# Performance work log

Measured on AMD Instinct MI355X. Metric: run time of the kernel, lower is better.

The kernel has to match this reference:

```python
import jax, jax.numpy as jnp
import numpy as np

B, N, E = 4, 4096, 16384
D, A_DIM = 256, 64
T, HALF, STEPS, NTYPES = 16, 8, 3, 50


def setup_inputs() -> dict:
    key = jax.random.key(0)
    ks = jax.random.split(key, 16)
    s = 0.02  # small init so repeated DxD matmuls stay stable over 3 steps
    return {
        "annotation_id": jax.random.randint(ks[0], (B, N), 0, NTYPES),
        "src": jax.random.randint(ks[1], (B, E), 0, N),
        "dst": jax.random.randint(ks[2], (B, E), 0, N),
        "etype": jax.random.randint(ks[3], (B, E), 0, HALF),
        "edge_embed": jax.random.normal(ks[4], (T, D * D), jnp.float32) * s,
        "edge_bias": jax.random.normal(ks[5], (T, D), jnp.float32) * s,
        "type_embed": jax.random.normal(ks[6], (NTYPES, A_DIM), jnp.float32) * s,
        "Wr": jax.random.normal(ks[7], (D, 3 * D), jnp.float32) * s,
        "br": jnp.zeros((D,), jnp.float32),
        "Wz": jax.random.normal(ks[8], (D, 3 * D), jnp.float32) * s,
        "bz": jnp.zeros((D,), jnp.float32),
        "Wh": jax.random.normal(ks[9], (D, 3 * D), jnp.float32) * s,
        "bh": jnp.zeros((D,), jnp.float32),
        "Wa": jax.random.normal(ks[10], (1, D + A_DIM), jnp.float32) * s,
        "ba": jnp.zeros((1,), jnp.float32),
        "Wo": jax.random.normal(ks[11], (1, D + A_DIM), jnp.float32) * s,
        "bo": jnp.zeros((1,), jnp.float32),
    }


def reference(annotation_id, src, dst, etype, edge_embed, edge_bias, type_embed,
              Wr, br, Wz, bz, Wh, bh, Wa, ba, Wo, bo):
    # annotation: typeEmbed[id-1] if id>0 else zeros  -> [B, N, A_DIM]
    ann = jnp.where((annotation_id > 0)[..., None],
                    type_embed[jnp.clip(annotation_id - 1, 0, NTYPES - 1)],
                    jnp.zeros((), type_embed.dtype))
    # prop_state: annotation zero-padded to state_dim  -> [B, N, D]
    h = jnp.concatenate([ann, jnp.zeros((B, N, D - A_DIM), ann.dtype)], axis=-1)
    W = edge_embed.reshape(T, D, D)  # per-edge-type DxD matrices

    def step(h):
        # type-major projection: apply every edge-type matrix to every node state
        # P[b, t, n, :] = W[t] @ h[b, n]   -> [B, T, N, D]
        P = jnp.einsum('tij,bnj->btni', W, h)

        def per_graph(Pg, s_, d_, e_):
            # a_out[j]        += W[e] @ h[neighbour] + b[e]
            # a_in[neighbour] += W[e+HALF] @ h[j]   + b[e+HALF]
            m_out = Pg[e_, d_] + edge_bias[e_]            # [E, D]
            m_in = Pg[e_ + HALF, s_] + edge_bias[e_ + HALF]
            a_out = jnp.zeros((N, D), h.dtype).at[s_].add(m_out)
            a_in = jnp.zeros((N, D), h.dtype).at[d_].add(m_in)
            return a_in, a_out

        a_in, a_out = jax.vmap(per_graph)(P, src, dst, etype)
        # GRU-style propagator (dropout_rate = 0 -> identity)
        a = jnp.concatenate([a_in, a_out, h], axis=-1)    # [B, N, 3D]
        r = jax.nn.sigmoid(a @ Wr.T + br)
        z = jax.nn.sigmoid(a @ Wz.T + bz)
        h_hat = jnp.tanh(jnp.concatenate([a_in, a_out, r * h], axis=-1) @ Wh.T + bh)
        return (1.0 - z) * h + z * h_hat

    for _ in range(STEPS):
        h = step(h)

    join = jnp.concatenate([h, ann], axis=-1)             # [B, N, D+A]
    atten = jax.nn.sigmoid(join @ Wa.T + ba)              # [B, N, 1]
    ou = jnp.tanh(join @ Wo.T + bo)                       # [B, N, 1]
    w_sum = jnp.sum((atten * ou).reshape(-1, N), axis=1)  # [B]
    return jax.nn.sigmoid(w_sum)
```

## Files before the change

kernel.cpp:

```cpp
#include <hip/hip_runtime.h>
#include <cstdint>

#define BB 4
#define NN 4096
#define EE 16384
#define DD 256
#define ADIM 64
#define TT 16
#define HALFE 8
#define STEPS 3
#define OSTRIDE 4160
#define MAXTILES 1088
#define MAXM (MAXTILES * 128)

typedef __attribute__((ext_vector_type(8))) short short8;
typedef __attribute__((ext_vector_type(4))) float f32x4;

__device__ __forceinline__ float sigmoidf_(float x) { return 1.0f / (1.0f + __expf(-x)); }

__device__ __forceinline__ unsigned short f2bf(float x) {
    unsigned u = __float_as_uint(x);
    u += 0x7fffu + ((u >> 16) & 1u);
    return (unsigned short)(u >> 16);
}
__device__ __forceinline__ float bf2f(unsigned short b) {
    return __uint_as_float(((unsigned)b) << 16);
}

__global__ void init_kernel(const int* __restrict__ ann_id,
                            const float* __restrict__ type_embed,
                            float* __restrict__ ann, float* __restrict__ h,
                            unsigned short* __restrict__ hbf,
                            unsigned short* __restrict__ Xbf) {
    int idx = blockIdx.x * 256 + threadIdx.x;
    int bn = idx >> 6, q = idx & 63;
    int id = ann_id[bn];
    float4 v = {0.f, 0.f, 0.f, 0.f};
    if (q < 16) {
        if (id > 0) v = ((const float4*)(type_embed + (size_t)(id - 1) * ADIM))[q];
        ((float4*)(ann + (size_t)bn * ADIM))[q] = v;
    }
    ((float4*)(h + (size_t)bn * DD))[q] = v;
    ushort4 o;
    o.x = f2bf(v.x); o.y = f2bf(v.y); o.z = f2bf(v.z); o.w = f2bf(v.w);
    ((ushort4*)(hbf + (size_t)bn * DD))[q] = o;
    ((ushort4*)(Xbf + (size_t)bn * 768 + 512))[q] = o;
}

__global__ void conv_f2b4(const float* __restrict__ in, unsigned short* __restrict__ out) {
    int idx = blockIdx.x * 256 + threadIdx.x;
    float4 v = ((const float4*)in)[idx];
    ushort4 o;
    o.x = f2bf(v.x); o.y = f2bf(v.y); o.z = f2bf(v.z); o.w = f2bf(v.w);
    ((ushort4*)out)[idx] = o;
}

__global__ void build_wcat(const float* __restrict__ Wr, const float* __restrict__ Wz,
                           const float* __restrict__ Wh, unsigned short* __restrict__ W) {
    int idx = blockIdx.x * 256 + threadIdx.x;
    int c = idx / 768, k = idx % 768;
    float v;
    if (c < 256)       v = Wr[c * 768 + k];
    else if (c < 512)  v = Wz[(c - 256) * 768 + k];
    else               v = (k < 512) ? Wh[(c - 512) * 768 + k] : 0.f;
    W[idx] = f2bf(v);
}

__global__ void build_whh(const float* __restrict__ Wh, unsigned short* __restrict__ W) {
    int idx = blockIdx.x * 256 + threadIdx.x;
    int i = idx / 256, k = idx % 256;
    W[idx] = f2bf(Wh[i * 768 + 512 + k]);
}

__global__ void count_kernel(const int* __restrict__ src, const int* __restrict__ dst,
                             int* __restrict__ counts) {
    int idx = blockIdx.x * 256 + threadIdx.x;
    int b = idx >> 14;
    atomicAdd(&counts[(b * 2 + 0) * NN + src[idx]], 1);
    atomicAdd(&counts[(b * 2 + 1) * NN + dst[idx]], 1);
}

__global__ __launch_bounds__(1024) void scan_kernel(const int* __restrict__ counts,
                                                    int* __restrict__ offs,
                                                    int* __restrict__ cursor) {
    __shared__ int lsum[1024];
    int t = threadIdx.x, seg = blockIdx.x;
    int4 v = ((const int4*)(counts + (size_t)seg * NN))[t];
    int s1 = v.x + v.y, s2 = s1 + v.z, s3 = s2 + v.w;
    lsum[t] = s3;
    __syncthreads();
    for (int off = 1; off < 1024; off <<= 1) {
        int tmp = (t >= off) ? lsum[t - off] : 0;
        __syncthreads();
        lsum[t] += tmp;
        __syncthreads();
    }
    int base = lsum[t] - s3;
    int* o = offs + (size_t)seg * OSTRIDE;
    o[4 * t] = base; o[4 * t + 1] = base + v.x; o[4 * t + 2] = base + s1; o[4 * t + 3] = base + s2;
    if (t == 1023) o[4096] = lsum[1023];
    int* c = cursor + (size_t)seg * NN;
    c[4 * t] = base; c[4 * t + 1] = base + v.x; c[4 * t + 2] = base + s1; c[4 * t + 3] = base + s2;
}

__global__ void count2_kernel(const int* __restrict__ et, int* __restrict__ c32) {
    __shared__ int cnt[32];
    int tid = threadIdx.x;
    if (tid < 32) cnt[tid] = 0;
    __syncthreads();
    int idx = blockIdx.x * 256 + tid;
    int b = idx >> 14;
    atomicAdd(&cnt[b * 8 + et[idx]], 1);
    __syncthreads();
    if (tid < 32) atomicAdd(&c32[tid], cnt[tid]);
}

__global__ void scan2_kernel(const int* __restrict__ c32, int* __restrict__ type_cursor,
                             int* __restrict__ tile_type) {
    __shared__ int pad[64];
    int t = threadIdx.x;
    int b = t >> 4, dir = (t >> 3) & 1, tt = t & 7;
    int cnt = c32[b * 8 + tt];
    int padded = ((cnt + 127) >> 7) << 7;
    pad[t] = padded;
    __syncthreads();
    int off = 0;
    for (int k = 0; k < t; ++k) off += pad[k];
    type_cursor[t] = off;
    int t16 = dir * 8 + tt;
    int tile0 = off >> 7;
    for (int k = 0; k < (padded >> 7); ++k) tile_type[tile0 + k] = t16;
}

__global__ void fill2_kernel(const int* __restrict__ src, const int* __restrict__ dst,
                             const int* __restrict__ et, int* __restrict__ type_cursor,
                             int* __restrict__ node_cursor, int* __restrict__ entries,
                             int* __restrict__ idx2) {
    __shared__ int cnt[64];
    __shared__ int bse[64];
    int tid = threadIdx.x;
    if (tid < 64) cnt[tid] = 0;
    __syncthreads();
    int idx = blockIdx.x * 256 + tid;
    int b = idx >> 14;
    int s = src[idx], d = dst[idx], t = et[idx];
    int bin0 = b * 16 + t;
    int bin1 = b * 16 + 8 + t;
    int r0 = atomicAdd(&cnt[bin0], 1);
    int r1 = atomicAdd(&cnt[bin1], 1);
    __syncthreads();
    if (tid < 64) bse[tid] = atomicAdd(&type_cursor[tid], cnt[tid]);
    __syncthreads();
    int p0 = bse[bin0] + r0;
    int p1 = bse[bin1] + r1;
    idx2[p0] = b * NN + d;
    idx2[p1] = b * NN + s;
    int q0 = atomicAdd(&node_cursor[(b * 2 + 0) * NN + s], 1);
    entries[(size_t)(b * 2 + 0) * EE + q0] = (p0 << 4) | t;
    int q1 = atomicAdd(&node_cursor[(b * 2 + 1) * NN + d], 1);
    entries[(size_t)(b * 2 + 1) * EE + q1] = (p1 << 4) | (t + 8);
}

#define GEMM_CORE64(A_, Bt_, K_)                                                        \
    const int tid = threadIdx.x;                                                        \
    const int wv = tid >> 6, lane = tid & 63;                                           \
    const int wr = wv >> 1, wc = wv & 1;                                                \
    const int lr = lane & 15, hi = lane >> 4, rx = lane & 7;                            \
    const int srow = wv * 8 + (lane >> 3);                                              \
    const int scol = ((lane & 7) ^ (lane >> 3)) << 3;                                   \
    const unsigned short* Ag = A_ + (size_t)(r0 + srow) * K_ + scol;                    \
    const unsigned short* Bg = Bt_ + (size_t)(c0 + srow) * K_ + scol;                   \
    char* AsW = (char*)As + wv * 1024;                                                  \
    char* BsW = (char*)Bs + wv * 1024;                                                  \
    f32x4 acc[4][4] = {};                                                               \
    for (int k0 = 0; k0 < K_; k0 += 64) {                                               \
        _Pragma("unroll")                                                               \
        for (int i = 0; i < 4; ++i) {                                                   \
            __builtin_amdgcn_global_load_lds(                                           \
                (const __attribute__((address_space(1))) void*)(Ag + (size_t)(i * 32) * K_ + k0), \
                (__attribute__((address_space(3))) void*)(AsW + i * 4096), 16, 0, 0);   \
            __builtin_amdgcn_global_load_lds(                                           \
                (const __attribute__((address_space(1))) void*)(Bg + (size_t)(i * 32) * K_ + k0), \
                (__attribute__((address_space(3))) void*)(BsW + i * 4096), 16, 0, 0);   \
        }                                                                               \
        __syncthreads();                                                                \
        _Pragma("unroll")                                                               \
        for (int kk = 0; kk < 2; ++kk) {                                                \
            short8 af[4], bfv[4];                                                       \
            _Pragma("unroll")                                                           \
            for (int m = 0; m < 4; ++m) {                                               \
                int R = wr * 64 + m * 16 + lr;                                          \
                af[m] = *(const short8*)((const char*)As + R * 128 + (((kk * 4 + hi) ^ rx) << 4)); \
            }                                                                           \
            _Pragma("unroll")                                                           \
            for (int n = 0; n < 4; ++n) {                                               \
                int R = wc * 64 + n * 16 + lr;                                          \
                bfv[n] = *(const short8*)((const char*)Bs + R * 128 + (((kk * 4 + hi) ^ rx) << 4)); \
            }                                                                           \
            _Pragma("unroll")                                                           \
            for (int m = 0; m < 4; ++m)                                                 \
                _Pragma("unroll")                                                       \
                for (int n = 0; n < 4; ++n)                                             \
                    acc[m][n] = __builtin_amdgcn_mfma_f32_16x16x32_bf16(bfv[n], af[m], acc[m][n], 0, 0, 0); \
        }                                                                               \
        __syncthreads();                                                                \
    }                                                                                   \
    const int erow = r0 + wr * 64 + lr;                                                 \
    const int ecol = c0 + wc * 64 + (hi << 2);

__global__ __launch_bounds__(256) void gemm_msgs(const unsigned short* __restrict__ A,
                                                 const unsigned short* __restrict__ W2,
                                                 const int* __restrict__ idx2,
                                                 const int* __restrict__ tile_type,
                                                 unsigned short* __restrict__ C) {
    __shared__ __align__(16) unsigned short As[128 * 64];
    __shared__ __align__(16) unsigned short Bs[128 * 64];
    const int bid = blockIdx.x;
    const int wg = (bid & 7) * (MAXTILES * 2 / 8) + (bid >> 3);
    const int by = wg >> 1, bx = wg & 1;
    const int t16 = tile_type[by];
    if (t16 < 0) return;
    const int r0 = by << 7, c0 = bx << 7;
    const int tid = threadIdx.x;
    const int wv = tid >> 6, lane = tid & 63;
    const int wr = wv >> 1, wc = wv & 1;
    const int lr = lane & 15, hi = lane >> 4, rx = lane & 7;
    const int srow = wv * 8 + (lane >> 3);
    const int scol = ((lane & 7) ^ (lane >> 3)) << 3;
    int ar[4];
#pragma unroll
    for (int i = 0; i < 4; ++i) ar[i] = idx2[r0 + srow + i * 32];
    const unsigned short* Bt = W2 + (size_t)t16 * (DD * DD);
    const unsigned short* Bg = Bt + (size_t)(c0 + srow) * DD + scol;
    char* AsW = (char*)As + wv * 1024;
    char* BsW = (char*)Bs + wv * 1024;
    f32x4 acc[4][4] = {};
    for (int k0 = 0; k0 < DD; k0 += 64) {
#pragma unroll
        for (int i = 0; i < 4; ++i) {
            __builtin_amdgcn_global_load_lds(
                (const __attribute__((address_space(1))) void*)(A + (size_t)ar[i] * DD + scol + k0),
                (__attribute__((address_space(3))) void*)(AsW + i * 4096), 16, 0, 0);
            __builtin_amdgcn_global_load_lds(
                (const __attribute__((address_space(1))) void*)(Bg + (size_t)(i * 32) * DD + k0),
                (__attribute__((address_space(3))) void*)(BsW + i * 4096), 16, 0, 0);
        }
        __syncthreads();
#pragma unroll
        for (int kk = 0; kk < 2; ++kk) {
            short8 af[4], bfv[4];
#pragma unroll
            for (int m = 0; m < 4; ++m) {
                int R = wr * 64 + m * 16 + lr;
                af[m] = *(const short8*)((const char*)As + R * 128 + (((kk * 4 + hi) ^ rx) << 4));
            }
#pragma unroll
            for (int n = 0; n < 4; ++n) {
                int R = wc * 64 + n * 16 + lr;
                bfv[n] = *(const short8*)((const char*)Bs + R * 128 + (((kk * 4 + hi) ^ rx) << 4));
            }
#pragma unroll
            for (int m = 0; m < 4; ++m)
#pragma unroll
                for (int n = 0; n < 4; ++n)
                    acc[m][n] = __builtin_amdgcn_mfma_f32_16x16x32_bf16(bfv[n], af[m], acc[m][n], 0, 0, 0);
        }
        __syncthreads();
    }
    const int erow = r0 + wr * 64 + lr;
    const int ecol = c0 + wc * 64 + (hi << 2);
#pragma unroll
    for (int m = 0; m < 4; ++m)
#pragma unroll
        for (int n = 0; n < 4; ++n) {
            ushort4 o;
            o.x = f2bf(acc[m][n][0]); o.y = f2bf(acc[m][n][1]);
            o.z = f2bf(acc[m][n][2]); o.w = f2bf(acc[m][n][3]);
            *(ushort4*)&C[(size_t)(erow + m * 16) * DD + ecol + n * 16] = o;
        }
}

__global__ __launch_bounds__(256) void gemm_rzu(const unsigned short* __restrict__ A,
                                                const unsigned short* __restrict__ Bt,
                                                const float* __restrict__ br,
                                                const float* __restrict__ bz,
                                                const float* __restrict__ h,
                                                unsigned short* __restrict__ RH,
                                                unsigned short* __restrict__ Zb,
                                                unsigned short* __restrict__ Ub) {
    __shared__ __align__(16) unsigned short As[128 * 64];
    __shared__ __align__(16) unsigned short Bs[128 * 64];
    const int bid = blockIdx.x;
    const int wg = (bid & 7) * 96 + (bid >> 3);
    const int bx = wg % 6, by = wg / 6;
    const int r0 = by << 7, c0 = bx << 7;
    GEMM_CORE64(A, Bt, 768)
    const int region = c0 >> 8;
#pragma unroll
    for (int m = 0; m < 4; ++m)
#pragma unroll
        for (int n = 0; n < 4; ++n) {
            int gr = erow + m * 16;
            int gc = ecol + n * 16;
            f32x4 v = acc[m][n];
            if (region == 0) {
                float4 bb = *(const float4*)&br[gc];
                float4 hv = *(const float4*)&h[(size_t)gr * 256 + gc];
                ushort4 o;
                o.x = f2bf(sigmoidf_(v[0] + bb.x) * hv.x);
                o.y = f2bf(sigmoidf_(v[1] + bb.y) * hv.y);
                o.z = f2bf(sigmoidf_(v[2] + bb.z) * hv.z);
                o.w = f2bf(sigmoidf_(v[3] + bb.w) * hv.w);
                *(ushort4*)&RH[(size_t)gr * 256 + gc] = o;
            } else if (region == 1) {
                int c = gc - 256;
                float4 bb = *(const float4*)&bz[c];
                ushort4 o;
                o.x = f2bf(sigmoidf_(v[0] + bb.x));
                o.y = f2bf(sigmoidf_(v[1] + bb.y));
                o.z = f2bf(sigmoidf_(v[2] + bb.z));
                o.w = f2bf(sigmoidf_(v[3] + bb.w));
                *(ushort4*)&Zb[(size_t)gr * 256 + c] = o;
            } else {
                int c = gc - 512;
                ushort4 o;
                o.x = f2bf(v[0]); o.y = f2bf(v[1]); o.z = f2bf(v[2]); o.w = f2bf(v[3]);
                *(ushort4*)&Ub[(size_t)gr * 256 + c] = o;
            }
        }
}

__global__ __launch_bounds__(256) void gemm_hh(const unsigned short* __restrict__ A,
                                               const unsigned short* __restrict__ Bt,
                                               const unsigned short* __restrict__ Zb,
                                               const unsigned short* __restrict__ Ub,
                                               const float* __restrict__ bh,
                                               float* __restrict__ h,
                                               unsigned short* __restrict__ hbf,
                                               unsigned short* __restrict__ Xbf) {
    __shared__ __align__(16) unsigned short As[128 * 64];
    __shared__ __align__(16) unsigned short Bs[128 * 64];
    const int bid = blockIdx.x;
    const int wg = (bid & 7) * 32 + (bid >> 3);
    const int bx = wg & 1, by = wg >> 1;
    const int r0 = by << 7, c0 = bx << 7;
    GEMM_CORE64(A, Bt, 256)
#pragma unroll
    for (int m = 0; m < 4; ++m)
#pragma unroll
        for (int n = 0; n < 4; ++n) {
            int gr = erow + m * 16;
            int gc = ecol + n * 16;
            size_t base = (size_t)gr * 256 + gc;
            f32x4 v = acc[m][n];
            float4 bb = *(const float4*)&bh[gc];
            float4 hv = *(const float4*)&h[base];
            ushort4 zp = *(const ushort4*)&Zb[base];
            ushort4 up = *(const ushort4*)&Ub[base];
            float4 hn;
            {
                float z = bf2f(zp.x); hn.x = (1.f - z) * hv.x + z * tanhf(bf2f(up.x) + v[0] + bb.x);
            }{
                float z = bf2f(zp.y); hn.y = (1.f - z) * hv.y + z * tanhf(bf2f(up.y) + v[1] + bb.y);
            }{
                float z = bf2f(zp.z); hn.z = (1.f - z) * hv.z + z * tanhf(bf2f(up.z) + v[2] + bb.z);
            }{
                float z = bf2f(zp.w); hn.w = (1.f - z) * hv.w + z * tanhf(bf2f(up.w) + v[3] + bb.w);
            }
            *(float4*)&h[base] = hn;
            ushort4 o;
            o.x = f2bf(hn.x); o.y = f2bf(hn.y); o.z = f2bf(hn.z); o.w = f2bf(hn.w);
            *(ushort4*)&hbf[base] = o;
            *(ushort4*)&Xbf[(size_t)gr * 768 + 512 + gc] = o;
        }
}

__global__ void gather2_kernel(const unsigned short* __restrict__ msgs,
                               const int* __restrict__ offs, const int* __restrict__ entries,
                               const float* __restrict__ bias, unsigned short* __restrict__ Xb) {
    int wv = threadIdx.x >> 6, lane = threadIdx.x & 63;
    int slot = blockIdx.x * 4 + wv;
    int b = slot >> 13;
    int dir = (slot >> 12) & 1;
    int node = slot & 4095;
    const int* o = offs + (size_t)(b * 2 + dir) * OSTRIDE;
    int beg = o[node], end = o[node + 1];
    const int* ent = entries + (size_t)(b * 2 + dir) * EE;
    const float4* bias4 = (const float4*)bias;
    float4 acc = {0.f, 0.f, 0.f, 0.f};
    for (int p = beg; p < end; ++p) {
        int e2 = ent[p];
        int row = e2 >> 4, t = e2 & 15;
        ushort4 pv = *(const ushort4*)(msgs + (size_t)row * DD + lane * 4);
        float4 bv = bias4[t * 64 + lane];
        acc.x += bf2f(pv.x) + bv.x;
        acc.y += bf2f(pv.y) + bv.y;
        acc.z += bf2f(pv.z) + bv.z;
        acc.w += bf2f(pv.w) + bv.w;
    }
    ushort4 o4;
    o4.x = f2bf(acc.x); o4.y = f2bf(acc.y); o4.z = f2bf(acc.z); o4.w = f2bf(acc.w);
    int colbase = (dir == 0 ? 256 : 0) + lane * 4;
    *(ushort4*)(Xb + ((size_t)b * NN + node) * 768 + colbase) = o4;
}

__global__ void final_reduce(const float* __restrict__ h, const float* __restrict__ ann,
                             const float* __restrict__ Wa, const float* __restrict__ ba,
                             const float* __restrict__ Wo, const float* __restrict__ bo,
                             float* __restrict__ acc) {
    int wv = threadIdx.x >> 6, lane = threadIdx.x & 63;
    int b = blockIdx.x >> 5;
    int nbase = (blockIdx.x & 31) * 128 + wv * 32;
    float4 wah = ((const float4*)Wa)[lane];
    float4 woh = ((const float4*)Wo)[lane];
    float4 waa = {0, 0, 0, 0}, woa = {0, 0, 0, 0};
    if (lane < 16) {
        waa = ((const float4*)(Wa + 256))[lane];
        woa = ((const float4*)(Wo + 256))[lane];
    }
    float bav = ba[0], bov = bo[0];
    float part = 0.f;
    for (int it = 0; it < 32; ++it) {
        int node = nbase + it;
        float4 hv = ((const float4*)(h + ((size_t)b * NN + node) * DD))[lane];
        float sa = hv.x * wah.x + hv.y * wah.y + hv.z * wah.z + hv.w * wah.w;
        float so = hv.x * woh.x + hv.y * woh.y + hv.z * woh.z + hv.w * woh.w;
        if (lane < 16) {
            float4 av = ((const float4*)(ann + ((size_t)b * NN + node) * ADIM))[lane];
            sa += av.x * waa.x + av.y * waa.y + av.z * waa.z + av.w * waa.w;
            so += av.x * woa.x + av.y * woa.y + av.z * woa.z + av.w * woa.w;
        }
        for (int off = 32; off; off >>= 1) {
            sa += __shfl_down(sa, off);
            so += __shfl_down(so, off);
        }
        if (lane == 0) part += sigmoidf_(sa + bav) * tanhf(so + bov);
    }
    if (lane == 0) atomicAdd(&acc[b], part);
}

__global__ void final_out(const float* __restrict__ acc, float* __restrict__ out) {
    int b = threadIdx.x;
    if (b < BB) out[b] = sigmoidf_(acc[b]);
}

extern "C" void kernel_launch(void* const* d_in, const int* in_sizes, int n_in,
                              void* d_out, int out_size, void* d_ws, size_t ws_size,
                              hipStream_t stream) {
    const int*   ann_id     = (const int*)d_in[0];
    const int*   src        = (const int*)d_in[1];
    const int*   dst        = (const int*)d_in[2];
    const int*   etype      = (const int*)d_in[3];
    const float* edge_embed = (const float*)d_in[4];
    const float* edge_bias  = (const float*)d_in[5];
    const float* type_embed = (const float*)d_in[6];
    const float* Wr = (const float*)d_in[7];
    const float* br = (const float*)d_in[8];
    const float* Wz = (const float*)d_in[9];
    const float* bz = (const float*)d_in[10];
    const float* Wh = (const float*)d_in[11];
    const float* bh = (const float*)d_in[12];
    const float* Wa = (const float*)d_in[13];
    const float* ba = (const float*)d_in[14];
    const float* Wo = (const float*)d_in[15];
    const float* bo = (const float*)d_in[16];
    float* out = (float*)d_out;

    char* base = (char*)d_ws;
    size_t off = 0;
    auto alloc = [&](size_t bytes) { char* p = base + off; off += (bytes + 255) & ~(size_t)255; return p; };
    float* ann  = (float*)alloc((size_t)BB * NN * ADIM * 4);
    float* h    = (float*)alloc((size_t)BB * NN * DD * 4);
    float* acc  = (float*)alloc(64);
    unsigned short* h_bf   = (unsigned short*)alloc((size_t)BB * NN * DD * 2);
    unsigned short* W2bf   = (unsigned short*)alloc((size_t)TT * DD * DD * 2);
    unsigned short* Wcatbf = (unsigned short*)alloc(768 * 768 * 2);
    unsigned short* Whhbf  = (unsigned short*)alloc(256 * 256 * 2);
    unsigned short* msgs   = (unsigned short*)alloc((size_t)MAXM * DD * 2);
    unsigned short* Xbf    = (unsigned short*)alloc((size_t)BB * NN * 768 * 2);
    unsigned short* RHbf   = (unsigned short*)alloc((size_t)BB * NN * DD * 2);
    unsigned short* Zb     = (unsigned short*)alloc((size_t)BB * NN * DD * 2);
    unsigned short* Ub     = (unsigned short*)alloc((size_t)BB * NN * DD * 2);
    int* counts  = (int*)alloc((size_t)BB * 2 * NN * 4);
    int* cursor  = (int*)alloc((size_t)BB * 2 * NN * 4);
    int* offsets = (int*)alloc((size_t)BB * 2 * OSTRIDE * 4);
    int* entries = (int*)alloc((size_t)BB * 2 * EE * 4);
    int* c32     = (int*)alloc(32 * 4);
    int* tcur    = (int*)alloc(64 * 4);
    int* ttype   = (int*)alloc(MAXTILES * 4);
    int* idx2    = (int*)alloc((size_t)MAXM * 4);

    init_kernel<<<dim3((BB * NN * 64) / 256), dim3(256), 0, stream>>>(
        ann_id, type_embed, ann, h, h_bf, Xbf);
    conv_f2b4<<<dim3((TT * DD * DD) / 1024), dim3(256), 0, stream>>>(edge_embed, W2bf);
    build_wcat<<<dim3((768 * 768) / 256), dim3(256), 0, stream>>>(Wr, Wz, Wh, Wcatbf);
    build_whh<<<dim3((256 * 256) / 256), dim3(256), 0, stream>>>(Wh, Whhbf);
    hipMemsetAsync(counts, 0, (size_t)BB * 2 * NN * 4, stream);
    hipMemsetAsync(c32, 0, 32 * 4, stream);
    hipMemsetAsync(ttype, 0xFF, MAXTILES * 4, stream);
    hipMemsetAsync(idx2, 0, (size_t)MAXM * 4, stream);
    count_kernel<<<dim3((BB * EE) / 256), dim3(256), 0, stream>>>(src, dst, counts);
    count2_kernel<<<dim3((BB * EE) / 256), dim3(256), 0, stream>>>(etype, c32);
    scan_kernel<<<dim3(BB * 2), dim3(1024), 0, stream>>>(counts, offsets, cursor);
    scan2_kernel<<<dim3(1), dim3(64), 0, stream>>>(c32, tcur, ttype);
    fill2_kernel<<<dim3((BB * EE) / 256), dim3(256), 0, stream>>>(
        src, dst, etype, tcur, cursor, entries, idx2);

    for (int s = 0; s < STEPS; ++s) {
        gemm_msgs<<<dim3(MAXTILES * 2), dim3(256), 0, stream>>>(
            h_bf, W2bf, idx2, ttype, msgs);
        gather2_kernel<<<dim3(BB * 2 * NN / 4), dim3(256), 0, stream>>>(
            msgs, offsets, entries, edge_bias, Xbf);
        gemm_rzu<<<dim3(768), dim3(256), 0, stream>>>(
            Xbf, Wcatbf, br, bz, h, RHbf, Zb, Ub);
        gemm_hh<<<dim3(256), dim3(256), 0, stream>>>(
            RHbf, Whhbf, Zb, Ub, bh, h, h_bf, Xbf);
    }

    hipMemsetAsync(acc, 0, 64, stream);
    final_reduce<<<dim3(128), dim3(256), 0, stream>>>(h, ann, Wa, ba, Wo, bo, acc);
    final_out<<<dim3(1), dim3(64), 0, stream>>>(acc, out);
}
```

Baseline: 442.6 us.

## Double-buffer LDS tiles in GEMM kernels to overlap global loads with MFMA

Shared-memory A and B tiles in the message GEMM and the GRU GEMMs are now double-buffered. The first k-slice is prefetched before the loop, and each iteration issues the async global-to-LDS loads for the next slice into the other buffer before running the MFMAs on the current one. This removes one barrier per iteration and hides load latency behind compute. In exchange, LDS use per block doubles to 64KB, which may reduce the number of blocks resident per CU.

```diff
diff --git a/kernel.cpp b/kernel.cpp
--- a/kernel.cpp
+++ b/kernel.cpp
@@ -12,6 +12,9 @@
 #define OSTRIDE 4160
 #define MAXTILES 1088
 #define MAXM (MAXTILES * 128)
+
+#define AS1 __attribute__((address_space(1)))
+#define AS3 __attribute__((address_space(3)))
 
 typedef __attribute__((ext_vector_type(8))) short short8;
 typedef __attribute__((ext_vector_type(4))) float f32x4;
@@ -161,7 +164,7 @@
     entries[(size_t)(b * 2 + 1) * EE + q1] = (p1 << 4) | (t + 8);
 }
 
-#define GEMM_CORE64(A_, Bt_, K_)                                                        \
+#define GEMM_CORE64_DB(A_, Bt_, K_)                                                     \
     const int tid = threadIdx.x;                                                        \
     const int wv = tid >> 6, lane = tid & 63;                                           \
     const int wr = wv >> 1, wc = wv & 1;                                                \
@@ -170,32 +173,44 @@
     const int scol = ((lane & 7) ^ (lane >> 3)) << 3;                                   \
     const unsigned short* Ag = A_ + (size_t)(r0 + srow) * K_ + scol;                    \
     const unsigned short* Bg = Bt_ + (size_t)(c0 + srow) * K_ + scol;                   \
-    char* AsW = (char*)As + wv * 1024;                                                  \
-    char* BsW = (char*)Bs + wv * 1024;                                                  \
     f32x4 acc[4][4] = {};                                                               \
-    for (int k0 = 0; k0 < K_; k0 += 64) {                                               \
-        _Pragma("unroll")                                                               \
-        for (int i = 0; i < 4; ++i) {                                                   \
-            __builtin_amdgcn_global_load_lds(                                           \
-                (const __attribute__((address_space(1))) void*)(Ag + (size_t)(i * 32) * K_ + k0), \
-                (__attribute__((address_space(3))) void*)(AsW + i * 4096), 16, 0, 0);   \
-            __builtin_amdgcn_global_load_lds(                                           \
-                (const __attribute__((address_space(1))) void*)(Bg + (size_t)(i * 32) * K_ + k0), \
-                (__attribute__((address_space(3))) void*)(BsW + i * 4096), 16, 0, 0);   \
+    _Pragma("unroll")                                                                   \
+    for (int i = 0; i < 4; ++i) {                                                       \
+        __builtin_amdgcn_global_load_lds(                                               \
+            (const AS1 void*)(Ag + (size_t)(i * 32) * K_),                              \
+            (AS3 void*)((char*)As + wv * 1024 + i * 4096), 16, 0, 0);                   \
+        __builtin_amdgcn_global_load_lds(                                               \
+            (const AS1 void*)(Bg + (size_t)(i * 32) * K_),                              \
+            (AS3 void*)((char*)Bs + wv * 1024 + i * 4096), 16, 0, 0);                   \
+    }                                                                                   \
+    __syncthreads();                                                                    \
+    for (int it = 0; it < K_ / 64; ++it) {                                              \
+        const int cb = (it & 1) << 14;                                                  \
+        if (it + 1 < K_ / 64) {                                                         \
+            const int pb = ((it + 1) & 1) << 14;                                        \
+            const int kof = (it + 1) * 64;                                              \
+            _Pragma("unroll")                                                           \
+            for (int i = 0; i < 4; ++i) {                                               \
+                __builtin_amdgcn_global_load_lds(                                       \
+                    (const AS1 void*)(Ag + (size_t)(i * 32) * K_ + kof),                \
+                    (AS3 void*)((char*)As + pb + wv * 1024 + i * 4096), 16, 0, 0);      \
+                __builtin_amdgcn_global_load_lds(                                       \
+                    (const AS1 void*)(Bg + (size_t)(i * 32) * K_ + kof),                \
+                    (AS3 void*)((char*)Bs + pb + wv * 1024 + i * 4096), 16, 0, 0);      \
+            }                                                                           \
         }                                                                               \
-        __syncthreads();                                                                \
         _Pragma("unroll")                                                               \
         for (int kk = 0; kk < 2; ++kk) {                                                \
             short8 af[4], bfv[4];                                                       \
             _Pragma("unroll")                                                           \
             for (int m = 0; m < 4; ++m) {                                               \
                 int R = wr * 64 + m * 16 + lr;                                          \
-                af[m] = *(const short8*)((const char*)As + R * 128 + (((kk * 4 + hi) ^ rx) << 4)); \
+                af[m] = *(const short8*)((const char*)As + cb + R * 128 + (((kk * 4 + hi) ^ rx) << 4)); \
             }                                                                           \
             _Pragma("unroll")                                                           \
             for (int n = 0; n < 4; ++n) {                                               \
                 int R = wc * 64 + n * 16 + lr;                                          \
-                bfv[n] = *(const short8*)((const char*)Bs + R * 128 + (((kk * 4 + hi) ^ rx) << 4)); \
+                bfv[n] = *(const short8*)((const char*)Bs + cb + R * 128 + (((kk * 4 + hi) ^ rx) << 4)); \
             }                                                                           \
             _Pragma("unroll")                                                           \
             for (int m = 0; m < 4; ++m)                                                 \
@@ -213,8 +228,8 @@
                                                  const int* __restrict__ idx2,
                                                  const int* __restrict__ tile_type,
                                                  unsigned short* __restrict__ C) {
-    __shared__ __align__(16) unsigned short As[128 * 64];
-    __shared__ __align__(16) unsigned short Bs[128 * 64];
+    __shared__ __align__(16) unsigned short As[2 * 128 * 64];
+    __shared__ __align__(16) unsigned short Bs[2 * 128 * 64];
     const int bid = blockIdx.x;
     const int wg = (bid & 7) * (MAXTILES * 2 / 8) + (bid >> 3);
     const int by = wg >> 1, bx = wg & 1;
@@ -232,32 +247,44 @@
     for (int i = 0; i < 4; ++i) ar[i] = idx2[r0 + srow + i * 32];
     const unsigned short* Bt = W2 + (size_t)t16 * (DD * DD);
     const unsigned short* Bg = Bt + (size_t)(c0 + srow) * DD + scol;
-    char* AsW = (char*)As + wv * 1024;
-    char* BsW = (char*)Bs + wv * 1024;
     f32x4 acc[4][4] = {};
-    for (int k0 = 0; k0 < DD; k0 += 64) {
-#pragma unroll
-        for (int i = 0; i < 4; ++i) {
-            __builtin_amdgcn_global_load_lds(
-                (const __attribute__((address_space(1))) void*)(A + (size_t)ar[i] * DD + scol + k0),
-                (__attribute__((address_space(3))) void*)(AsW + i * 4096), 16, 0, 0);
-            __builtin_amdgcn_global_load_lds(
-                (const __attribute__((address_space(1))) void*)(Bg + (size_t)(i * 32) * DD + k0),
-                (__attribute__((address_space(3))) void*)(BsW + i * 4096), 16, 0, 0);
-        }
-        __syncthreads();
+#pragma unroll
+    for (int i = 0; i < 4; ++i) {
+        __builtin_amdgcn_global_load_lds(
+            (const AS1 void*)(A + (size_t)ar[i] * DD + scol),
+            (AS3 void*)((char*)As + wv * 1024 + i * 4096), 16, 0, 0);
+        __builtin_amdgcn_global_load_lds(
+            (const AS1 void*)(Bg + (size_t)(i * 32) * DD),
+            (AS3 void*)((char*)Bs + wv * 1024 + i * 4096), 16, 0, 0);
+    }
+    __syncthreads();
+    for (int it = 0; it < DD / 64; ++it) {
+        const int cb = (it & 1) << 14;
+        if (it + 1 < DD / 64) {
+            const int pb = ((it + 1) & 1) << 14;
+            const int kof = (it + 1) * 64;
+#pragma unroll
+            for (int i = 0; i < 4; ++i) {
+                __builtin_amdgcn_global_load_lds(
+                    (const AS1 void*)(A + (size_t)ar[i] * DD + scol + kof),
+                    (AS3 void*)((char*)As + pb + wv * 1024 + i * 4096), 16, 0, 0);
+                __builtin_amdgcn_global_load_lds(
+                    (const AS1 void*)(Bg + (size_t)(i * 32) * DD + kof),
+                    (AS3 void*)((char*)Bs + pb + wv * 1024 + i * 4096), 16, 0, 0);
+            }
+        }
 #pragma unroll
         for (int kk = 0; kk < 2; ++kk) {
             short8 af[4], bfv[4];
 #pragma unroll
             for (int m = 0; m < 4; ++m) {
                 int R = wr * 64 + m * 16 + lr;
-                af[m] = *(const short8*)((const char*)As + R * 128 + (((kk * 4 + hi) ^ rx) << 4));
+                af[m] = *(const short8*)((const char*)As + cb + R * 128 + (((kk * 4 + hi) ^ rx) << 4));
             }
 #pragma unroll
             for (int n = 0; n < 4; ++n) {
                 int R = wc * 64 + n * 16 + lr;
-                bfv[n] = *(const short8*)((const char*)Bs + R * 128 + (((kk * 4 + hi) ^ rx) << 4));
+                bfv[n] = *(const short8*)((const char*)Bs + cb + R * 128 + (((kk * 4 + hi) ^ rx) << 4));
             }
 #pragma unroll
             for (int m = 0; m < 4; ++m)
@@ -288,13 +315,13 @@
                                                 unsigned short* __restrict__ RH,
                                                 unsigned short* __restrict__ Zb,
                                                 unsigned short* __restrict__ Ub) {
-    __shared__ __align__(16) unsigned short As[128 * 64];
-    __shared__ __align__(16) unsigned short Bs[128 * 64];
+    __shared__ __align__(16) unsigned short As[2 * 128 * 64];
+    __shared__ __align__(16) unsigned short Bs[2 * 128 * 64];
     const int bid = blockIdx.x;
     const int wg = (bid & 7) * 96 + (bid >> 3);
     const int bx = wg % 6, by = wg / 6;
     const int r0 = by << 7, c0 = bx << 7;
-    GEMM_CORE64(A, Bt, 768)
+    GEMM_CORE64_DB(A, Bt, 768)
     const int region = c0 >> 8;
 #pragma unroll
     for (int m = 0; m < 4; ++m)
@@ -338,13 +365,13 @@
                                                float* __restrict__ h,
                                                unsigned short* __restrict__ hbf,
                                                unsigned short* __restrict__ Xbf) {
-    __shared__ __align__(16) unsigned short As[128 * 64];
-    __shared__ __align__(16) unsigned short Bs[128 * 64];
+    __shared__ __align__(16) unsigned short As[2 * 128 * 64];
+    __shared__ __align__(16) unsigned short Bs[2 * 128 * 64];
     const int bid = blockIdx.x;
     const int wg = (bid & 7) * 32 + (bid >> 3);
     const int bx = wg & 1, by = wg >> 1;
     const int r0 = by << 7, c0 = bx << 7;
-    GEMM_CORE64(A, Bt, 256)
+    GEMM_CORE64_DB(A, Bt, 256)
 #pragma unroll
     for (int m = 0; m < 4; ++m)
 #pragma unroll
```

Measured after the change: 465.7 us. 5.2% more time.
